# Kernel optimization log

Measured on AMD Instinct MI355X. Metric: run time of the kernel, lower is better.

The kernel has to match this reference:

```python
import jax, jax.numpy as jnp
import numpy as np

HEADS = 4
NEG = -1e30


def layer_norm(x, g, b, eps=1e-5):
    m = x.mean(-1, keepdims=True)
    v = ((x - m) ** 2).mean(-1, keepdims=True)
    return (x - m) / jnp.sqrt(v + eps) * g + b


def setup_inputs() -> dict:
    key = jax.random.key(0)
    B, S, H, V, L = 16, 512, 1024, 8000, 8
    ks = jax.random.split(key, 12)
    inp = {}
    inp['x'] = jax.random.randint(ks[0], (B, S), 0, V)
    inp['lengths'] = jax.random.randint(ks[1], (B,), 4, S + 1)
    inp['emb'] = jax.random.normal(ks[2], (V, H), jnp.float32) * 0.02
    inp['Wq'] = jax.random.normal(ks[3], (L, H, H), jnp.float32) * 0.02
    inp['bq'] = jnp.zeros((L, H), jnp.float32)
    inp['Wk'] = jax.random.normal(ks[4], (L, H, H), jnp.float32) * 0.02
    inp['bk'] = jnp.zeros((L, H), jnp.float32)
    inp['Wv'] = jax.random.normal(ks[5], (L, H, H), jnp.float32) * 0.02
    inp['bv'] = jnp.zeros((L, H), jnp.float32)
    inp['W1'] = jax.random.normal(ks[6], (L, H, H), jnp.float32) * 0.02
    inp['b1'] = jnp.zeros((L, H), jnp.float32)
    inp['W2'] = jax.random.normal(ks[7], (L, H, H), jnp.float32) * 0.02
    inp['b2'] = jnp.zeros((L, H), jnp.float32)
    inp['g1'] = jnp.ones((L, H), jnp.float32)
    inp['be1'] = jnp.zeros((L, H), jnp.float32)
    inp['g2'] = jnp.ones((L, H), jnp.float32)
    inp['be2'] = jnp.zeros((L, H), jnp.float32)
    inp['Wfc'] = jax.random.normal(ks[8], (H, H), jnp.float32) * 0.02
    inp['bfc'] = jnp.zeros((H,), jnp.float32)
    return inp


def reference(x, lengths, emb, Wq, bq, Wk, bk, Wv, bv, W1, b1, W2, b2, g1, be1, g2, be2, Wfc, bfc):
    B, S = x.shape
    V, H = emb.shape
    dh = H // HEADS
    L = Wq.shape[0]
    # token embedding + sinusoidal positional encoding
    pos = jnp.arange(S, dtype=jnp.float32)[:, None]
    div = jnp.exp(jnp.arange(0, H, 2, dtype=jnp.float32) * (-np.log(10000.0) / H))
    pe = jnp.zeros((S, H), jnp.float32)
    pe = pe.at[:, 0::2].set(jnp.sin(pos * div)).at[:, 1::2].set(jnp.cos(pos * div))
    z = emb[x] + pe[None]
    # masks: causal + padding on queries + (faithful source quirk) head index < length
    i = jnp.arange(S)
    causal = i[None, :] <= i[:, None]                                   # [S,S]
    q_valid = i[None, :] < lengths[:, None]                             # [B,S]
    h_valid = jnp.arange(HEADS)[None, :] < lengths[:, None]             # [B,HEADS]
    row_valid = q_valid[:, None, :, None] & h_valid[:, :, None, None]   # [B,HEADS,S,1]
    mask = causal[None, None] & row_valid                               # [B,HEADS,S,S]
    scale = 1.0 / np.sqrt(H)  # faithful: scales by sqrt(HIDDEN), not head dim
    atten_last = None
    for l in range(L):
        q = (z @ Wq[l].T + bq[l]).reshape(B, S, HEADS, dh).transpose(0, 2, 1, 3)
        k = (z @ Wk[l].T + bk[l]).reshape(B, S, HEADS, dh).transpose(0, 2, 1, 3)
        v = (z @ Wv[l].T + bv[l]).reshape(B, S, HEADS, dh).transpose(0, 2, 1, 3)
        s = jnp.einsum('bhqd,bhkd->bhqk', q, k) * scale
        p = jax.nn.softmax(jnp.where(mask, s, NEG), axis=-1)
        p = jnp.where(row_valid, p, 0.0)  # zero fully-masked rows (source's atten>0 trick)
        o = jnp.einsum('bhqk,bhkd->bhqd', p, v)
        # faithful source bug: reshape [B,HEADS,S,dh] -> [B,S,H] WITHOUT transposing heads back
        o = o.reshape(B, S, H)
        atten_last = p.max(axis=-1)  # [B,HEADS,S]
        z1 = layer_norm(z + o, g1[l], be1[l])
        f = jax.nn.gelu(z1 @ W1[l].T + b1[l], approximate=False) @ W2[l].T + b2[l]
        z = layer_norm(z1 + f, g2[l], be2[l])
    out_fc = z @ Wfc.T + bfc
    logits = out_fc @ emb.T  # tied output projection
    y_prim = jax.nn.softmax(logits, axis=-1)
    return y_prim, atten_last
```

## Files before the change

### kernel.cpp

```cpp
#include <hip/hip_runtime.h>
#include <math.h>


typedef unsigned short u16;
typedef unsigned int u32;
typedef __attribute__((ext_vector_type(8))) short short8;
typedef __attribute__((ext_vector_type(4))) float f32x4;

__device__ __forceinline__ u16 f2bf(float f) {
    u32 u = __builtin_bit_cast(u32, f);
    u32 r = (u + 0x7FFFu + ((u >> 16) & 1u)) >> 16;
    return (u16)r;
}
__device__ __forceinline__ float bf2f(u16 u) {
    u32 v = ((u32)u) << 16;
    return __builtin_bit_cast(float, v);
}
__device__ __forceinline__ float4 unpack4(uint2 r) {
    float4 f;
    f.x = __builtin_bit_cast(float, r.x << 16);
    f.y = __builtin_bit_cast(float, r.x & 0xffff0000u);
    f.z = __builtin_bit_cast(float, r.y << 16);
    f.w = __builtin_bit_cast(float, r.y & 0xffff0000u);
    return f;
}

__device__ __forceinline__ void stage16(const void* g, void* ldsbase, int lane) {
#if __has_builtin(__builtin_amdgcn_global_load_lds)
    __builtin_amdgcn_global_load_lds(
        (const __attribute__((address_space(1))) u32*)g,
        (__attribute__((address_space(3))) u32*)ldsbase, 16, 0, 0);
#else
    *(short8*)((u16*)ldsbase + lane * 8) = *(const short8*)g;
#endif
}

__global__ __launch_bounds__(256) void gemm_bf16(
    const u16* __restrict__ A, const u16* __restrict__ B,
    const float* __restrict__ bias, void* __restrict__ C,
    int M, int N, int K, int ldc, int Nstore, int flags,
    u16* __restrict__ VtOut)
{
    __shared__ u16 As[128 * 64];
    __shared__ u16 Bs[128 * 64];
    const int tid = threadIdx.x;
    const int w = tid >> 6, lane = tid & 63;
    const int m0 = blockIdx.y * 128, n0 = blockIdx.x * 128;
    const int lr = lane >> 3;
    const int lc = lane & 7;
    f32x4 acc[4][4];
#pragma unroll
    for (int i = 0; i < 4; ++i)
#pragma unroll
        for (int j = 0; j < 4; ++j) {
            acc[i][j][0] = 0.f; acc[i][j][1] = 0.f;
            acc[i][j][2] = 0.f; acc[i][j][3] = 0.f;
        }
    const int row = lane & 15, quad = lane >> 4;
    const int wm = (w >> 1) * 64, wn = (w & 1) * 64;

    for (int k0 = 0; k0 < K; k0 += 64) {
        __syncthreads();
#pragma unroll
        for (int i = 0; i < 4; ++i) {
            const int ra = (w * 4 + i) * 8 + lr;
            const int ca = lc ^ (ra & 7);
            stage16(A + (size_t)(m0 + ra) * K + k0 + ca * 8, &As[(w * 4 + i) * 512], lane);
            stage16(B + (size_t)(n0 + ra) * K + k0 + ca * 8, &Bs[(w * 4 + i) * 512], lane);
        }
        __syncthreads();
#pragma unroll
        for (int kk = 0; kk < 2; ++kk) {
            const int g0 = kk * 4 + quad;
            short8 af[4], bfr[4];
#pragma unroll
            for (int i = 0; i < 4; ++i) {
                const int r = wm + i * 16 + row;
                af[i] = *(const short8*)&As[r * 64 + ((g0 ^ (r & 7)) * 8)];
            }
#pragma unroll
            for (int j = 0; j < 4; ++j) {
                const int r = wn + j * 16 + row;
                bfr[j] = *(const short8*)&Bs[r * 64 + ((g0 ^ (r & 7)) * 8)];
            }
#pragma unroll
            for (int i = 0; i < 4; ++i)
#pragma unroll
                for (int j = 0; j < 4; ++j)
                    acc[i][j] = __builtin_amdgcn_mfma_f32_16x16x32_bf16(
                        af[i], bfr[j], acc[i][j], 0, 0, 0);
        }
    }
    const int do_bf = flags & 1, do_gelu = flags & 2, do_qkv = flags & 4;
#pragma unroll
    for (int i = 0; i < 4; ++i)
#pragma unroll
        for (int j = 0; j < 4; ++j) {
            const int gr0 = m0 + wm + i * 16 + quad * 4;
            const int gc = n0 + wn + j * 16 + row;
            if (gc < Nstore) {
                const float bv = bias ? bias[gc] : 0.f;
                if (do_qkv && gc >= 2048) {
                    const int d = gc - 2048;
                    const int bb = gr0 >> 9, s = gr0 & 511;
                    ushort4 ov;
                    ov.x = f2bf(acc[i][j][0] + bv);
                    ov.y = f2bf(acc[i][j][1] + bv);
                    ov.z = f2bf(acc[i][j][2] + bv);
                    ov.w = f2bf(acc[i][j][3] + bv);
                    *(ushort4*)(VtOut +
                        (((size_t)(bb * 4 + (d >> 8)) * 256 + (d & 255)) * 512 + s)) = ov;
                } else {
#pragma unroll
                    for (int r = 0; r < 4; ++r) {
                        float v = acc[i][j][r] + bv;
                        if (do_gelu) v = 0.5f * v * (1.f + erff(v * 0.7071067811865475f));
                        if (do_bf) ((u16*)C)[(size_t)(gr0 + r) * ldc + gc] = f2bf(v);
                        else       ((float*)C)[(size_t)(gr0 + r) * ldc + gc] = v;
                    }
                }
            }
        }
}

__global__ __launch_bounds__(256, 2) void attn_mfma(
    const u16* __restrict__ QK, const u16* __restrict__ Vt,
    const int* __restrict__ lengths,
    float* __restrict__ O, float* __restrict__ atten)
{
    __shared__ u16 sK[64 * 256];
    __shared__ u16 sV[256 * 64];
    __shared__ u16 sP[4][16 * 64];
    const int qt = blockIdx.x, h = blockIdx.y, b = blockIdx.z;
    const int q0 = qt * 64;
    const int t = threadIdx.x;
    const int w = t >> 6, lane = t & 63;
    const int row = lane & 15, quad = lane >> 4;

    {
        const u16* qbase = QK + (size_t)(b * 512 + q0) * 2048 + h * 256;
        const int r2 = lane >> 5, c = lane & 31;
#pragma unroll
        for (int i = 0; i < 8; ++i) {
            const int rr = w * 16 + i * 2 + r2;
            stage16(qbase + (size_t)rr * 2048 + ((c ^ (rr & 7)) * 8),
                    &sK[(w * 16 + i * 2) * 256], lane);
        }
    }
    __syncthreads();
    short8 qf[8];
    {
        const int qr = w * 16 + row;
#pragma unroll
        for (int ds = 0; ds < 8; ++ds) {
            const int chunk = ds * 4 + quad;
            qf[ds] = *(const short8*)&sK[qr * 256 + ((chunk ^ (qr & 7)) * 8)];
        }
    }
    __syncthreads();

    float mrow[4], lrow[4];
#pragma unroll
    for (int j = 0; j < 4; ++j) { mrow[j] = -3.0e38f; lrow[j] = 0.f; }
    f32x4 oacc[16];
#pragma unroll
    for (int dt = 0; dt < 16; ++dt) {
        oacc[dt][0] = 0.f; oacc[dt][1] = 0.f; oacc[dt][2] = 0.f; oacc[dt][3] = 0.f;
    }

    const int nkt = qt + 1;
    for (int kt = 0; kt < nkt; ++kt) {
        const int k0 = kt * 64;
        {
            const u16* kbase = QK + (size_t)(b * 512 + k0) * 2048 + 1024 + h * 256;
            const int r2 = lane >> 5, c = lane & 31;
#pragma unroll
            for (int i = 0; i < 8; ++i) {
                const int rr = w * 16 + i * 2 + r2;
                stage16(kbase + (size_t)rr * 2048 + ((c ^ (rr & 7)) * 8),
                        &sK[(w * 16 + i * 2) * 256], lane);
            }
            const u16* vbase = Vt + ((size_t)(b * 4 + h) * 256) * 512 + k0;
            const int vr = lane >> 3, vc = lane & 7;
#pragma unroll
            for (int i = 0; i < 8; ++i) {
                const int dd = w * 64 + i * 8 + vr;
                stage16(vbase + (size_t)dd * 512 + ((vc ^ (dd & 7)) * 8),
                        &sV[(w * 64 + i * 8) * 64], lane);
            }
        }
        __syncthreads();

        f32x4 sacc[4];
#pragma unroll
        for (int kt4 = 0; kt4 < 4; ++kt4) {
            sacc[kt4][0] = 0.f; sacc[kt4][1] = 0.f;
            sacc[kt4][2] = 0.f; sacc[kt4][3] = 0.f;
        }
#pragma unroll
        for (int ds = 0; ds < 8; ++ds) {
            const int chunk = ds * 4 + quad;
#pragma unroll
            for (int kt4 = 0; kt4 < 4; ++kt4) {
                const int kr = kt4 * 16 + row;
                const short8 kf = *(const short8*)&sK[kr * 256 + ((chunk ^ (kr & 7)) * 8)];
                sacc[kt4] = __builtin_amdgcn_mfma_f32_16x16x32_bf16(
                    qf[ds], kf, sacc[kt4], 0, 0, 0);
            }
        }

        const int diag = (kt == qt);
        float sc[4][4];
#pragma unroll
        for (int kt4 = 0; kt4 < 4; ++kt4)
#pragma unroll
            for (int j = 0; j < 4; ++j) {
                float v = sacc[kt4][j] * 0.03125f;
                if (diag && (kt4 * 16 + row > w * 16 + quad * 4 + j)) v = -3.0e38f;
                sc[kt4][j] = v;
            }
        float alpha[4];
#pragma unroll
        for (int j = 0; j < 4; ++j) {
            float lm = fmaxf(fmaxf(sc[0][j], sc[1][j]), fmaxf(sc[2][j], sc[3][j]));
            lm = fmaxf(lm, __shfl_xor(lm, 1));
            lm = fmaxf(lm, __shfl_xor(lm, 2));
            lm = fmaxf(lm, __shfl_xor(lm, 4));
            lm = fmaxf(lm, __shfl_xor(lm, 8));
            const float mnew = fmaxf(mrow[j], lm);
            alpha[j] = __expf(mrow[j] - mnew);
            float ps = 0.f;
#pragma unroll
            for (int kt4 = 0; kt4 < 4; ++kt4) {
                sc[kt4][j] = __expf(sc[kt4][j] - mnew);
                ps += sc[kt4][j];
            }
            ps += __shfl_xor(ps, 1);
            ps += __shfl_xor(ps, 2);
            ps += __shfl_xor(ps, 4);
            ps += __shfl_xor(ps, 8);
            lrow[j] = lrow[j] * alpha[j] + ps;
            mrow[j] = mnew;
        }
#pragma unroll
        for (int kt4 = 0; kt4 < 4; ++kt4)
#pragma unroll
            for (int j = 0; j < 4; ++j) {
                const int ql = quad * 4 + j;
                const int k = kt4 * 16 + row;
                sP[w][ql * 64 + (((k >> 3) ^ (ql & 7)) * 8) + (k & 7)] = f2bf(sc[kt4][j]);
            }
#pragma unroll
        for (int dt = 0; dt < 16; ++dt) {
            oacc[dt][0] *= alpha[0]; oacc[dt][1] *= alpha[1];
            oacc[dt][2] *= alpha[2]; oacc[dt][3] *= alpha[3];
        }
#pragma unroll
        for (int kk = 0; kk < 2; ++kk) {
            const int chunk = kk * 4 + quad;
            const short8 pf = *(const short8*)&sP[w][row * 64 + ((chunk ^ (row & 7)) * 8)];
#pragma unroll
            for (int dt = 0; dt < 16; ++dt) {
                const int dr = dt * 16 + row;
                const short8 vf = *(const short8*)&sV[dr * 64 + ((chunk ^ (dr & 7)) * 8)];
                oacc[dt] = __builtin_amdgcn_mfma_f32_16x16x32_bf16(
                    pf, vf, oacc[dt], 0, 0, 0);
            }
        }
        __syncthreads();
    }

    const int len = lengths[b];
#pragma unroll
    for (int j = 0; j < 4; ++j) {
        const int qg = q0 + w * 16 + quad * 4 + j;
        const float linv = (qg < len) ? 1.f / lrow[j] : 0.f;
        float* op = O + ((size_t)((b * 4 + h) * 512 + qg)) * 256;
#pragma unroll
        for (int dt = 0; dt < 16; ++dt)
            op[dt * 16 + row] = oacc[dt][j] * linv;
        if (atten && row == 0)
            atten[(size_t)(b * 4 + h) * 512 + qg] = linv;
    }
}

__global__ __launch_bounds__(256) void embed_kernel(
    const int* __restrict__ x, const float* __restrict__ emb,
    float* __restrict__ Z, u16* __restrict__ Zb)
{
    const int tokidx = blockIdx.x;
    const int s = tokidx & 511;
    const int t = threadIdx.x;
    const int tok = x[tokidx];
    const int c0 = t << 2;
    float4 e = *(const float4*)(emb + (size_t)tok * 1024 + c0);
    float pe[4];
#pragma unroll
    for (int j = 0; j < 4; ++j) {
        int c = c0 + j;
        float freq = expf((float)(c & ~1) * (-9.210340371976184f / 1024.f));
        float arg = (float)s * freq;
        pe[j] = (c & 1) ? cosf(arg) : sinf(arg);
    }
    float4 o = make_float4(e.x + pe[0], e.y + pe[1], e.z + pe[2], e.w + pe[3]);
    *(float4*)(Z + (size_t)tokidx * 1024 + c0) = o;
    ushort4 ob = {f2bf(o.x), f2bf(o.y), f2bf(o.z), f2bf(o.w)};
    ((ushort4*)(Zb + (size_t)tokidx * 1024))[t] = ob;
}

__global__ __launch_bounds__(256) void add_ln(
    const float* __restrict__ X, const float* __restrict__ R,
    const float* __restrict__ g, const float* __restrict__ be,
    float* __restrict__ Y, u16* __restrict__ Yb)
{
    __shared__ float red[8];
    const int row = blockIdx.x;
    const int t = threadIdx.x;
    const float4 x = ((const float4*)(X + (size_t)row * 1024))[t];
    const float4 r = ((const float4*)(R + (size_t)row * 1024))[t];
    float v[4] = {x.x + r.x, x.y + r.y, x.z + r.z, x.w + r.w};
    float s = v[0] + v[1] + v[2] + v[3];
#pragma unroll
    for (int off = 32; off; off >>= 1) s += __shfl_xor(s, off);
    const int wid = t >> 6;
    if ((t & 63) == 0) red[wid] = s;
    __syncthreads();
    s = red[0] + red[1] + red[2] + red[3];
    const float mean = s * (1.f / 1024.f);
    float q = 0.f;
#pragma unroll
    for (int j = 0; j < 4; ++j) { float d = v[j] - mean; q += d * d; }
#pragma unroll
    for (int off = 32; off; off >>= 1) q += __shfl_xor(q, off);
    if ((t & 63) == 0) red[4 + wid] = q;
    __syncthreads();
    q = red[4] + red[5] + red[6] + red[7];
    const float rstd = rsqrtf(q * (1.f / 1024.f) + 1e-5f);
    const float4 gv = ((const float4*)g)[t];
    const float4 bv = ((const float4*)be)[t];
    float4 o;
    o.x = (v[0] - mean) * rstd * gv.x + bv.x;
    o.y = (v[1] - mean) * rstd * gv.y + bv.y;
    o.z = (v[2] - mean) * rstd * gv.z + bv.z;
    o.w = (v[3] - mean) * rstd * gv.w + bv.w;
    ((float4*)(Y + (size_t)row * 1024))[t] = o;
    ushort4 ob = {f2bf(o.x), f2bf(o.y), f2bf(o.z), f2bf(o.w)};
    ((ushort4*)(Yb + (size_t)row * 1024))[t] = ob;
}

__global__ __launch_bounds__(256) void softmax8000(float* __restrict__ P)
{
    __shared__ float red[8];
    float* p = P + (size_t)blockIdx.x * 8000;
    const int t = threadIdx.x;
    float vals[32];
    float mx = -3.0e38f;
#pragma unroll
    for (int j = 0; j < 32; ++j) {
        int c = t + (j << 8);
        if (c < 8000) { vals[j] = p[c]; mx = fmaxf(mx, vals[j]); }
    }
#pragma unroll
    for (int off = 32; off; off >>= 1) mx = fmaxf(mx, __shfl_xor(mx, off));
    const int wid = t >> 6;
    if ((t & 63) == 0) red[wid] = mx;
    __syncthreads();
    mx = fmaxf(fmaxf(red[0], red[1]), fmaxf(red[2], red[3]));
    float sum = 0.f;
#pragma unroll
    for (int j = 0; j < 32; ++j) {
        int c = t + (j << 8);
        if (c < 8000) { vals[j] = expf(vals[j] - mx); sum += vals[j]; }
    }
#pragma unroll
    for (int off = 32; off; off >>= 1) sum += __shfl_xor(sum, off);
    if ((t & 63) == 0) red[4 + wid] = sum;
    __syncthreads();
    const float inv = 1.f / (red[4] + red[5] + red[6] + red[7]);
#pragma unroll
    for (int j = 0; j < 32; ++j) {
        int c = t + (j << 8);
        if (c < 8000) p[c] = vals[j] * inv;
    }
}

__global__ __launch_bounds__(256) void cvt_qkv(
    const float* __restrict__ Wq, const float* __restrict__ Wk,
    const float* __restrict__ Wv, u16* __restrict__ dst)
{
    const int n = blockIdx.x, l = blockIdx.y, t = threadIdx.x;
    const float* src = (n < 1024) ? Wq + ((size_t)l * 1024 + n) * 1024
                     : (n < 2048) ? Wk + ((size_t)l * 1024 + (n - 1024)) * 1024
                                  : Wv + ((size_t)l * 1024 + (n - 2048)) * 1024;
    float4 v = ((const float4*)src)[t];
    ushort4 o = {f2bf(v.x), f2bf(v.y), f2bf(v.z), f2bf(v.w)};
    ((ushort4*)(dst + ((size_t)l * 3072 + n) * 1024))[t] = o;
}

__global__ __launch_bounds__(256) void cvt_bias_qkv(
    const float* __restrict__ bq, const float* __restrict__ bk,
    const float* __restrict__ bv, float* __restrict__ dst)
{
    const int i = blockIdx.x * 256 + threadIdx.x;
    if (i >= 8 * 3072) return;
    const int l = i / 3072, n = i - l * 3072;
    float v = (n < 1024) ? bq[l * 1024 + n]
            : (n < 2048) ? bk[l * 1024 + (n - 1024)]
                         : bv[l * 1024 + (n - 2048)];
    dst[i] = v;
}

__global__ __launch_bounds__(256) void cvt_plain(
    const float* __restrict__ src, u16* __restrict__ dst, int n)
{
    const int i = (blockIdx.x * 256 + threadIdx.x) * 4;
    if (i >= n) return;
    float4 v = *(const float4*)(src + i);
    ushort4 o = {f2bf(v.x), f2bf(v.y), f2bf(v.z), f2bf(v.w)};
    *(ushort4*)(dst + i) = o;
}

__global__ __launch_bounds__(256) void cvt_emb(
    const float* __restrict__ emb, u16* __restrict__ dst)
{
    const int r = blockIdx.x, t = threadIdx.x;
    ushort4 o = {0, 0, 0, 0};
    if (r < 8000) {
        float4 v = ((const float4*)(emb + (size_t)r * 1024))[t];
        o.x = f2bf(v.x); o.y = f2bf(v.y); o.z = f2bf(v.z); o.w = f2bf(v.w);
    }
    ((ushort4*)(dst + (size_t)r * 1024))[t] = o;
}

extern "C" void kernel_launch(void* const* d_in, const int* in_sizes, int n_in,
                              void* d_out, int out_size, void* d_ws, size_t ws_size,
                              hipStream_t stream)
{
    (void)in_sizes; (void)n_in; (void)out_size;
    const int*   x       = (const int*)d_in[0];
    const int*   lengths = (const int*)d_in[1];
    const float* emb = (const float*)d_in[2];
    const float* Wq  = (const float*)d_in[3];
    const float* bq  = (const float*)d_in[4];
    const float* Wk  = (const float*)d_in[5];
    const float* bk  = (const float*)d_in[6];
    const float* Wv  = (const float*)d_in[7];
    const float* bv  = (const float*)d_in[8];
    const float* W1  = (const float*)d_in[9];
    const float* b1  = (const float*)d_in[10];
    const float* W2  = (const float*)d_in[11];
    const float* b2  = (const float*)d_in[12];
    const float* g1  = (const float*)d_in[13];
    const float* be1 = (const float*)d_in[14];
    const float* g2  = (const float*)d_in[15];
    const float* be2 = (const float*)d_in[16];
    const float* Wfc = (const float*)d_in[17];
    const float* bfc = (const float*)d_in[18];

    float* out = (float*)d_out;
    float* atten = out + (size_t)65536000;

    const size_t SZ_EMBB = (size_t)8064 * 1024 * 2;
    const size_t SZ_FCB  = (size_t)8192 * 1024 * 2;
    const size_t SZ_BQKV = (size_t)8 * 3072 * 4;
    const size_t SZ_WQKV = (size_t)8 * 3072 * 1024 * 2;
    const size_t SZ_W12  = (size_t)8 * 1024 * 1024 * 2;
    const size_t SZ_WFC  = (size_t)1024 * 1024 * 2;
    const size_t SZ_Z    = (size_t)8192 * 1024 * 4;
    const size_t SZ_ZB   = (size_t)8192 * 1024 * 2;
    const size_t SZ_QKB  = (size_t)8192 * 2048 * 2;
    const size_t SZ_VT   = (size_t)16 * 4 * 256 * 512 * 2;
    const size_t NONFORCED = SZ_WQKV + 2 * SZ_W12 + SZ_WFC + 2 * SZ_Z + SZ_ZB
                           + SZ_QKB + SZ_VT + SZ_Z;
    const size_t FORCED = SZ_EMBB + SZ_FCB + SZ_BQKV;
    const size_t GRAND = FORCED + NONFORCED;

    char* wsc = (char*)d_ws;
    char* oc  = (char*)d_out;
    const size_t ocap = (size_t)65536000 * 4;
    size_t wo = 0, oo = 0;
    const bool all_ws = ws_size >= GRAND;
    u16*   emb_bf = (u16*)(wsc + wo);  wo += SZ_EMBB;
    u16*   fc_b   = (u16*)(wsc + wo);  wo += SZ_FCB;
    float* bqkv   = (float*)(wsc + wo); wo += SZ_BQKV;
    auto alloc = [&](size_t sz) -> char* {
        if (all_ws) { char* p = wsc + wo; wo += sz; return p; }
        if (oo + sz <= ocap) { char* p = oc + oo; oo += sz; return p; }
        char* p = wsc + wo; wo += sz; return p;
    };
    u16*   Wqkv_bf = (u16*)alloc(SZ_WQKV);
    u16*   W1b     = (u16*)alloc(SZ_W12);
    u16*   W2b     = (u16*)alloc(SZ_W12);
    u16*   Wfcb    = (u16*)alloc(SZ_WFC);
    float* z       = (float*)alloc(SZ_Z);
    float* z1      = (float*)alloc(SZ_Z);
    u16*   zb      = (u16*)alloc(SZ_ZB);
    u16*   qkb     = (u16*)alloc(SZ_QKB);
    u16*   vtb     = (u16*)alloc(SZ_VT);
    float* o       = (float*)alloc(SZ_Z);
    u16* z1b = qkb;
    u16* f1b = qkb + (size_t)8192 * 1024;

    dim3 blk(256);
    cvt_qkv<<<dim3(3072, 8), blk, 0, stream>>>(Wq, Wk, Wv, Wqkv_bf);
    cvt_bias_qkv<<<96, blk, 0, stream>>>(bq, bk, bv, bqkv);
    cvt_plain<<<8192, blk, 0, stream>>>(W1, W1b, 8 * 1024 * 1024);
    cvt_plain<<<8192, blk, 0, stream>>>(W2, W2b, 8 * 1024 * 1024);
    cvt_plain<<<1024, blk, 0, stream>>>(Wfc, Wfcb, 1024 * 1024);
    cvt_emb<<<8064, blk, 0, stream>>>(emb, emb_bf);

    embed_kernel<<<8192, blk, 0, stream>>>(x, emb, z, zb);

    for (int l = 0; l < 8; ++l) {
        const size_t WO1 = (size_t)l * 1024 * 1024;
        const size_t BO = (size_t)l * 1024;
        gemm_bf16<<<dim3(24, 64), blk, 0, stream>>>(
            zb, Wqkv_bf + (size_t)l * 3072 * 1024, bqkv + (size_t)l * 3072,
            qkb, 8192, 3072, 1024, 2048, 3072, 1 | 4, vtb);
        attn_mfma<<<dim3(8, 4, 16), blk, 0, stream>>>(
            qkb, vtb, lengths, o, (l == 7) ? atten : nullptr);
        add_ln<<<8192, blk, 0, stream>>>(z, o, g1 + BO, be1 + BO, z1, z1b);
        gemm_bf16<<<dim3(8, 64), blk, 0, stream>>>(
            z1b, W1b + WO1, b1 + BO, f1b, 8192, 1024, 1024, 1024, 1024, 1 | 2, nullptr);
        gemm_bf16<<<dim3(8, 64), blk, 0, stream>>>(
            f1b, W2b + WO1, b2 + BO, o, 8192, 1024, 1024, 1024, 1024, 0, nullptr);
        add_ln<<<8192, blk, 0, stream>>>(z1, o, g2 + BO, be2 + BO, z, zb);
    }
    gemm_bf16<<<dim3(8, 64), blk, 0, stream>>>(
        zb, Wfcb, bfc, fc_b, 8192, 1024, 1024, 1024, 1024, 1, nullptr);
    gemm_bf16<<<dim3(63, 64), blk, 0, stream>>>(
        fc_b, emb_bf, nullptr, out, 8192, 8064, 1024, 8000, 8000, 0, nullptr);
    softmax8000<<<8192, blk, 0, stream>>>(out);
}
```

Baseline: 2.801 ms.

## Rewrite GEMM with 128x256 tiles, triple-buffered async LDS staging, and XCD swizzle

Replaces the GEMM kernel with one that uses 128x256 output tiles and K-steps of 32. It keeps three LDS buffers, prefetching two steps ahead and waiting on explicit vmcnt counts, so global loads overlap with MFMA work. It also remaps block IDs so neighbouring tiles spread across XCDs, and raises wave priority around the MFMA bursts. The tied-embedding buffer is padded to 8192 rows to fit the wider tile, at the cost of a larger accumulator footprint and register pressure.

```diff
diff --git a/kernel.cpp b/kernel.cpp
--- a/kernel.cpp
+++ b/kernel.cpp
@@ -35,69 +35,122 @@
 #endif
 }
 
-__global__ __launch_bounds__(256) void gemm_bf16(
+__global__ __launch_bounds__(256, 2) void gemm_v2(
     const u16* __restrict__ A, const u16* __restrict__ B,
     const float* __restrict__ bias, void* __restrict__ C,
     int M, int N, int K, int ldc, int Nstore, int flags,
     u16* __restrict__ VtOut)
 {
-    __shared__ u16 As[128 * 64];
-    __shared__ u16 Bs[128 * 64];
+    __shared__ u16 As[3][128 * 32];
+    __shared__ u16 Bs[3][256 * 32];
     const int tid = threadIdx.x;
     const int w = tid >> 6, lane = tid & 63;
-    const int m0 = blockIdx.y * 128, n0 = blockIdx.x * 128;
-    const int lr = lane >> 3;
-    const int lc = lane & 7;
-    f32x4 acc[4][4];
-#pragma unroll
-    for (int i = 0; i < 4; ++i)
+    const int nwg = gridDim.x * gridDim.y;
+    int bid = blockIdx.y * gridDim.x + blockIdx.x;
+    if ((nwg & 7) == 0) bid = (bid & 7) * (nwg >> 3) + (bid >> 3);
+    const int n0 = (bid % gridDim.x) * 256;
+    const int m0 = (bid / gridDim.x) * 128;
+
+    const int srow = lane >> 2;
+    const int sslot = lane & 3;
+#define SW(r) (((r) & 3) ^ (((r) >> 2) & 3))
+
+    const u16* Abase = A + (size_t)m0 * K;
+    const u16* Bbase = B + (size_t)n0 * K;
+
+    auto stageA = [&](int buf, int kt) {
+        const int k0 = kt * 32;
+#pragma unroll
+        for (int i = 0; i < 2; ++i) {
+            const int rbase = w * 32 + i * 16;
+            const int r = rbase + srow;
+            const int g = sslot ^ SW(r);
+            stage16(Abase + (size_t)r * K + k0 + g * 8, &As[buf][rbase * 32], lane);
+        }
+    };
+    auto stageB = [&](int buf, int kt) {
+        const int k0 = kt * 32;
+#pragma unroll
+        for (int i = 0; i < 4; ++i) {
+            const int rbase = w * 64 + i * 16;
+            const int r = rbase + srow;
+            const int g = sslot ^ SW(r);
+            stage16(Bbase + (size_t)r * K + k0 + g * 8, &Bs[buf][rbase * 32], lane);
+        }
+    };
+
+    f32x4 acc[8][4];
+#pragma unroll
+    for (int i = 0; i < 8; ++i)
 #pragma unroll
         for (int j = 0; j < 4; ++j) {
             acc[i][j][0] = 0.f; acc[i][j][1] = 0.f;
             acc[i][j][2] = 0.f; acc[i][j][3] = 0.f;
         }
-    const int row = lane & 15, quad = lane >> 4;
-    const int wm = (w >> 1) * 64, wn = (w & 1) * 64;
-
-    for (int k0 = 0; k0 < K; k0 += 64) {
-        __syncthreads();
+    const int col = lane & 15, quad = lane >> 4;
+    const int wn = w * 64;
+    const int nt = K >> 5;
+
+    stageA(0, 0); stageB(0, 0);
+    stageA(1, 1); stageB(1, 1);
+
+    int buf = 0;
+    for (int t = 0; t < nt; ++t) {
+        __builtin_amdgcn_s_barrier();
+        if (t + 2 < nt) {
+            int b2 = buf + 2; if (b2 >= 3) b2 -= 3;
+            stageA(b2, t + 2); stageB(b2, t + 2);
+            asm volatile("s_waitcnt vmcnt(12)" ::: "memory");
+        } else if (t + 1 < nt) {
+            asm volatile("s_waitcnt vmcnt(6)" ::: "memory");
+        } else {
+            asm volatile("s_waitcnt vmcnt(0)" ::: "memory");
+        }
+        __builtin_amdgcn_s_barrier();
+        __builtin_amdgcn_sched_barrier(0);
+
+        short8 bf4[4], af4[4];
+#pragma unroll
+        for (int j = 0; j < 4; ++j) {
+            const int r = wn + j * 16 + col;
+            bf4[j] = *(const short8*)&Bs[buf][r * 32 + ((quad ^ SW(r)) * 8)];
+        }
 #pragma unroll
         for (int i = 0; i < 4; ++i) {
-            const int ra = (w * 4 + i) * 8 + lr;
-            const int ca = lc ^ (ra & 7);
-            stage16(A + (size_t)(m0 + ra) * K + k0 + ca * 8, &As[(w * 4 + i) * 512], lane);
-            stage16(B + (size_t)(n0 + ra) * K + k0 + ca * 8, &Bs[(w * 4 + i) * 512], lane);
-        }
-        __syncthreads();
-#pragma unroll
-        for (int kk = 0; kk < 2; ++kk) {
-            const int g0 = kk * 4 + quad;
-            short8 af[4], bfr[4];
-#pragma unroll
-            for (int i = 0; i < 4; ++i) {
-                const int r = wm + i * 16 + row;
-                af[i] = *(const short8*)&As[r * 64 + ((g0 ^ (r & 7)) * 8)];
-            }
-#pragma unroll
-            for (int j = 0; j < 4; ++j) {
-                const int r = wn + j * 16 + row;
-                bfr[j] = *(const short8*)&Bs[r * 64 + ((g0 ^ (r & 7)) * 8)];
-            }
-#pragma unroll
-            for (int i = 0; i < 4; ++i)
-#pragma unroll
-                for (int j = 0; j < 4; ++j)
-                    acc[i][j] = __builtin_amdgcn_mfma_f32_16x16x32_bf16(
-                        af[i], bfr[j], acc[i][j], 0, 0, 0);
-        }
-    }
+            const int r = i * 16 + col;
+            af4[i] = *(const short8*)&As[buf][r * 32 + ((quad ^ SW(r)) * 8)];
+        }
+        __builtin_amdgcn_s_setprio(1);
+#pragma unroll
+        for (int i = 0; i < 4; ++i)
+#pragma unroll
+            for (int j = 0; j < 4; ++j)
+                acc[i][j] = __builtin_amdgcn_mfma_f32_16x16x32_bf16(
+                    af4[i], bf4[j], acc[i][j], 0, 0, 0);
+        __builtin_amdgcn_s_setprio(0);
+#pragma unroll
+        for (int i = 0; i < 4; ++i) {
+            const int r = (4 + i) * 16 + col;
+            af4[i] = *(const short8*)&As[buf][r * 32 + ((quad ^ SW(r)) * 8)];
+        }
+        __builtin_amdgcn_s_setprio(1);
+#pragma unroll
+        for (int i = 0; i < 4; ++i)
+#pragma unroll
+            for (int j = 0; j < 4; ++j)
+                acc[4 + i][j] = __builtin_amdgcn_mfma_f32_16x16x32_bf16(
+                    af4[i], bf4[j], acc[4 + i][j], 0, 0, 0);
+        __builtin_amdgcn_s_setprio(0);
+        buf = buf + 1; if (buf >= 3) buf -= 3;
+    }
+
     const int do_bf = flags & 1, do_gelu = flags & 2, do_qkv = flags & 4;
 #pragma unroll
-    for (int i = 0; i < 4; ++i)
+    for (int i = 0; i < 8; ++i)
 #pragma unroll
         for (int j = 0; j < 4; ++j) {
-            const int gr0 = m0 + wm + i * 16 + quad * 4;
-            const int gc = n0 + wn + j * 16 + row;
+            const int gr0 = m0 + i * 16 + quad * 4;
+            const int gc = n0 + wn + j * 16 + col;
             if (gc < Nstore) {
                 const float bv = bias ? bias[gc] : 0.f;
                 if (do_qkv && gc >= 2048) {
@@ -121,6 +174,7 @@
                 }
             }
         }
+#undef SW
 }
 
 __global__ __launch_bounds__(256, 2) void attn_mfma(
@@ -460,7 +514,7 @@
     float* out = (float*)d_out;
     float* atten = out + (size_t)65536000;
 
-    const size_t SZ_EMBB = (size_t)8064 * 1024 * 2;
+    const size_t SZ_EMBB = (size_t)8192 * 1024 * 2;
     const size_t SZ_FCB  = (size_t)8192 * 1024 * 2;
     const size_t SZ_BQKV = (size_t)8 * 3072 * 4;
     const size_t SZ_WQKV = (size_t)8 * 3072 * 1024 * 2;
@@ -507,28 +561,28 @@
     cvt_plain<<<8192, blk, 0, stream>>>(W1, W1b, 8 * 1024 * 1024);
     cvt_plain<<<8192, blk, 0, stream>>>(W2, W2b, 8 * 1024 * 1024);
     cvt_plain<<<1024, blk, 0, stream>>>(Wfc, Wfcb, 1024 * 1024);
-    cvt_emb<<<8064, blk, 0, stream>>>(emb, emb_bf);
+    cvt_emb<<<8192, blk, 0, stream>>>(emb, emb_bf);
 
     embed_kernel<<<8192, blk, 0, stream>>>(x, emb, z, zb);
 
     for (int l = 0; l < 8; ++l) {
         const size_t WO1 = (size_t)l * 1024 * 1024;
         const size_t BO = (size_t)l * 1024;
-        gemm_bf16<<<dim3(24, 64), blk, 0, stream>>>(
+        gemm_v2<<<dim3(12, 64), blk, 0, stream>>>(
             zb, Wqkv_bf + (size_t)l * 3072 * 1024, bqkv + (size_t)l * 3072,
             qkb, 8192, 3072, 1024, 2048, 3072, 1 | 4, vtb);
         attn_mfma<<<dim3(8, 4, 16), blk, 0, stream>>>(
             qkb, vtb, lengths, o, (l == 7) ? atten : nullptr);
         add_ln<<<8192, blk, 0, stream>>>(z, o, g1 + BO, be1 + BO, z1, z1b);
-        gemm_bf16<<<dim3(8, 64), blk, 0, stream>>>(
+        gemm_v2<<<dim3(4, 64), blk, 0, stream>>>(
             z1b, W1b + WO1, b1 + BO, f1b, 8192, 1024, 1024, 1024, 1024, 1 | 2, nullptr);
-        gemm_bf16<<<dim3(8, 64), blk, 0, stream>>>(
+        gemm_v2<<<dim3(4, 64), blk, 0, stream>>>(
             f1b, W2b + WO1, b2 + BO, o, 8192, 1024, 1024, 1024, 1024, 0, nullptr);
         add_ln<<<8192, blk, 0, stream>>>(z1, o, g2 + BO, be2 + BO, z, zb);
     }
-    gemm_bf16<<<dim3(8, 64), blk, 0, stream>>>(
+    gemm_v2<<<dim3(4, 64), blk, 0, stream>>>(
         zb, Wfcb, bfc, fc_b, 8192, 1024, 1024, 1024, 1024, 1, nullptr);
-    gemm_bf16<<<dim3(63, 64), blk, 0, stream>>>(
-        fc_b, emb_bf, nullptr, out, 8192, 8064, 1024, 8000, 8000, 0, nullptr);
+    gemm_v2<<<dim3(32, 64), blk, 0, stream>>>(
+        fc_b, emb_bf, nullptr, out, 8192, 8192, 1024, 8000, 8000, 0, nullptr);
     softmax8000<<<8192, blk, 0, stream>>>(out);
 }
```

New measurement: 3.339 ms. 1.19x slower.

## Double-buffer GEMM LDS tiles with async prefetch and XCD-aware block remap

Applied to the files above, without the earlier changes.

Turns the bf16 GEMM into a two-stage pipeline. Two LDS buffers let the global-to-LDS loads for tile t+2 be issued while MFMAs consume tile t, and partial vmcnt waits replace the full sync pairs. Block IDs are remapped across the 8 XCDs for better L2 locality, and setprio raises wave priority around the MFMA section. LDS use doubles to 64KB per block under a 2-blocks-per-CU launch bound, and the vmcnt(8) count relies on each stage issuing exactly 8 loads.

```diff
diff --git a/kernel.cpp b/kernel.cpp
--- a/kernel.cpp
+++ b/kernel.cpp
@@ -35,19 +35,38 @@
 #endif
 }
 
-__global__ __launch_bounds__(256) void gemm_bf16(
+__global__ __launch_bounds__(256, 2) void gemm_p(
     const u16* __restrict__ A, const u16* __restrict__ B,
     const float* __restrict__ bias, void* __restrict__ C,
     int M, int N, int K, int ldc, int Nstore, int flags,
     u16* __restrict__ VtOut)
 {
-    __shared__ u16 As[128 * 64];
-    __shared__ u16 Bs[128 * 64];
+    __shared__ u16 As[2][128 * 64];
+    __shared__ u16 Bs[2][128 * 64];
     const int tid = threadIdx.x;
     const int w = tid >> 6, lane = tid & 63;
-    const int m0 = blockIdx.y * 128, n0 = blockIdx.x * 128;
+    const int nwg = gridDim.x * gridDim.y;
+    int bid = blockIdx.y * gridDim.x + blockIdx.x;
+    if ((nwg & 7) == 0) bid = (bid & 7) * (nwg >> 3) + (bid >> 3);
+    const int n0 = (bid % gridDim.x) * 128;
+    const int m0 = (bid / gridDim.x) * 128;
+
     const int lr = lane >> 3;
     const int lc = lane & 7;
+
+    auto stages = [&](int buf, int kt) {
+        const int k0 = kt * 64;
+#pragma unroll
+        for (int i = 0; i < 4; ++i) {
+            const int ra = (w * 4 + i) * 8 + lr;
+            const int ca = lc ^ (ra & 7);
+            stage16(A + (size_t)(m0 + ra) * K + k0 + ca * 8,
+                    &As[buf][(w * 4 + i) * 512], lane);
+            stage16(B + (size_t)(n0 + ra) * K + k0 + ca * 8,
+                    &Bs[buf][(w * 4 + i) * 512], lane);
+        }
+    };
+
     f32x4 acc[4][4];
 #pragma unroll
     for (int i = 0; i < 4; ++i)
@@ -58,17 +77,17 @@
         }
     const int row = lane & 15, quad = lane >> 4;
     const int wm = (w >> 1) * 64, wn = (w & 1) * 64;
-
-    for (int k0 = 0; k0 < K; k0 += 64) {
-        __syncthreads();
-#pragma unroll
-        for (int i = 0; i < 4; ++i) {
-            const int ra = (w * 4 + i) * 8 + lr;
-            const int ca = lc ^ (ra & 7);
-            stage16(A + (size_t)(m0 + ra) * K + k0 + ca * 8, &As[(w * 4 + i) * 512], lane);
-            stage16(B + (size_t)(n0 + ra) * K + k0 + ca * 8, &Bs[(w * 4 + i) * 512], lane);
-        }
-        __syncthreads();
+    const int nt = K >> 6;
+
+    stages(0, 0);
+    if (nt > 1) stages(1, 1);
+
+    for (int t = 0; t < nt; ++t) {
+        if (t + 1 < nt) asm volatile("s_waitcnt vmcnt(8)" ::: "memory");
+        else            asm volatile("s_waitcnt vmcnt(0)" ::: "memory");
+        __builtin_amdgcn_s_barrier();
+        __builtin_amdgcn_sched_barrier(0);
+        const int buf = t & 1;
 #pragma unroll
         for (int kk = 0; kk < 2; ++kk) {
             const int g0 = kk * 4 + quad;
@@ -76,21 +95,27 @@
 #pragma unroll
             for (int i = 0; i < 4; ++i) {
                 const int r = wm + i * 16 + row;
-                af[i] = *(const short8*)&As[r * 64 + ((g0 ^ (r & 7)) * 8)];
+                af[i] = *(const short8*)&As[buf][r * 64 + ((g0 ^ (r & 7)) * 8)];
             }
 #pragma unroll
             for (int j = 0; j < 4; ++j) {
                 const int r = wn + j * 16 + row;
-                bfr[j] = *(const short8*)&Bs[r * 64 + ((g0 ^ (r & 7)) * 8)];
-            }
+                bfr[j] = *(const short8*)&Bs[buf][r * 64 + ((g0 ^ (r & 7)) * 8)];
+            }
+            __builtin_amdgcn_s_setprio(1);
 #pragma unroll
             for (int i = 0; i < 4; ++i)
 #pragma unroll
                 for (int j = 0; j < 4; ++j)
                     acc[i][j] = __builtin_amdgcn_mfma_f32_16x16x32_bf16(
                         af[i], bfr[j], acc[i][j], 0, 0, 0);
-        }
-    }
+            __builtin_amdgcn_s_setprio(0);
+        }
+        __builtin_amdgcn_sched_barrier(0);
+        __builtin_amdgcn_s_barrier();
+        if (t + 2 < nt) stages(buf, t + 2);
+    }
+
     const int do_bf = flags & 1, do_gelu = flags & 2, do_qkv = flags & 4;
 #pragma unroll
     for (int i = 0; i < 4; ++i)
@@ -514,21 +539,21 @@
     for (int l = 0; l < 8; ++l) {
         const size_t WO1 = (size_t)l * 1024 * 1024;
         const size_t BO = (size_t)l * 1024;
-        gemm_bf16<<<dim3(24, 64), blk, 0, stream>>>(
+        gemm_p<<<dim3(24, 64), blk, 0, stream>>>(
             zb, Wqkv_bf + (size_t)l * 3072 * 1024, bqkv + (size_t)l * 3072,
             qkb, 8192, 3072, 1024, 2048, 3072, 1 | 4, vtb);
         attn_mfma<<<dim3(8, 4, 16), blk, 0, stream>>>(
             qkb, vtb, lengths, o, (l == 7) ? atten : nullptr);
         add_ln<<<8192, blk, 0, stream>>>(z, o, g1 + BO, be1 + BO, z1, z1b);
-        gemm_bf16<<<dim3(8, 64), blk, 0, stream>>>(
+        gemm_p<<<dim3(8, 64), blk, 0, stream>>>(
             z1b, W1b + WO1, b1 + BO, f1b, 8192, 1024, 1024, 1024, 1024, 1 | 2, nullptr);
-        gemm_bf16<<<dim3(8, 64), blk, 0, stream>>>(
+        gemm_p<<<dim3(8, 64), blk, 0, stream>>>(
             f1b, W2b + WO1, b2 + BO, o, 8192, 1024, 1024, 1024, 1024, 0, nullptr);
         add_ln<<<8192, blk, 0, stream>>>(z1, o, g2 + BO, be2 + BO, z, zb);
     }
-    gemm_bf16<<<dim3(8, 64), blk, 0, stream>>>(
+    gemm_p<<<dim3(8, 64), blk, 0, stream>>>(
         zb, Wfcb, bfc, fc_b, 8192, 1024, 1024, 1024, 1024, 1, nullptr);
-    gemm_bf16<<<dim3(63, 64), blk, 0, stream>>>(
+    gemm_p<<<dim3(63, 64), blk, 0, stream>>>(
         fc_b, emb_bf, nullptr, out, 8192, 8064, 1024, 8000, 8000, 0, nullptr);
     softmax8000<<<8192, blk, 0, stream>>>(out);
 }
```

Result: no change. 2.759 ms (-1.5%).
